# Kernel tuning notes

Hardware: AMD Instinct MI355X
Metric: run time of the kernel (lower is better)

The kernel has to match this reference:

```python
import jax, jax.numpy as jnp
import numpy as np

B, L, H = 32, 512, 1024
H2 = H // 2          # split half = 512
D_ATTN = 64
EPS = 1e-5


def setup_inputs() -> dict:
    key = jax.random.key(0)
    ks = jax.random.split(key, 6)
    x = jax.random.normal(ks[0], (B, L, H), dtype=jnp.float32)
    # LayerNorm params (default torch init: weight=1, bias=0)
    ln_gamma = jnp.ones((H2,), jnp.float32)
    ln_beta = jnp.zeros((H2,), jnp.float32)
    # Toeplitz params (module inits w_vector=0, bias=1; use small random w for nontrivial math)
    w_vector = jax.random.normal(ks[1], (2 * L - 1,), jnp.float32) * 0.02
    t_bias = jnp.ones((L,), jnp.float32)
    # TinyAttention: kqv Linear(H2 -> 3*d_attn), proj Linear(d_attn -> H2)
    kqv_w = jax.random.normal(ks[2], (H2, 3 * D_ATTN), jnp.float32) * 0.02
    kqv_b = jnp.zeros((3 * D_ATTN,), jnp.float32)
    proj_w = jax.random.normal(ks[3], (D_ATTN, H2), jnp.float32) * 0.02
    proj_b = jnp.zeros((H2,), jnp.float32)
    return {"x": x, "ln_gamma": ln_gamma, "ln_beta": ln_beta,
            "w_vector": w_vector, "t_bias": t_bias,
            "kqv_w": kqv_w, "kqv_b": kqv_b, "proj_w": proj_w, "proj_b": proj_b}


def _toeplitz(w_vector):
    # Faithful replication of get_toeplitz(): pad, tile, trim, reshape, crop.
    r = w_vector.shape[0] // 2            # = L - 1
    t = jnp.pad(w_vector, (0, L))         # length 3L - 1
    t = jnp.tile(t, L)[:-L]               # length L * (3L - 2)
    t = t.reshape(L, 3 * L - 2)
    return t[:, r:-r]                      # [L, L]


def _tiny_attention(v, kqv_w, kqv_b, proj_w, proj_b):
    kqv = v @ kqv_w + kqv_b                        # [B, L, 3*d_attn]
    k, q, val = jnp.split(kqv, 3, axis=-1)         # chunk order: key, query, value
    scale = 1.0 / jnp.sqrt(jnp.float32(q.shape[-1]))
    scores = jnp.einsum('bqd,bkd->bqk', q, k) * scale
    soft = jax.nn.softmax(scores, axis=-1)
    head = jnp.einsum('bqk,bkd->bqd', soft, val)   # [B, L, d_attn]
    return head @ proj_w + proj_b                  # [B, L, H2]


def reference(x, ln_gamma, ln_beta, w_vector, t_bias, kqv_w, kqv_b, proj_w, proj_b):
    u, v = jnp.split(x, 2, axis=-1)                # each [B, L, H2]
    head = _tiny_attention(v, kqv_w, kqv_b, proj_w, proj_b)
    # LayerNorm over last dim
    mu = jnp.mean(v, axis=-1, keepdims=True)
    var = jnp.mean(jnp.square(v - mu), axis=-1, keepdims=True)
    vn = (v - mu) * jax.lax.rsqrt(var + EPS) * ln_gamma + ln_beta
    # spatial (Toeplitz) mixing: permute -> [B, H2, L], matmul [L, L], bias
    w_t = _toeplitz(w_vector)
    vm = jnp.einsum('blc,lm->bmc', vn, w_t.T).transpose(0, 2, 1)  # keep faithful: vp @ w_t
    vm = jnp.einsum('bcl,lm->bcm', vn.transpose(0, 2, 1), w_t) + t_bias
    v_out = vm.transpose(0, 2, 1) + head           # [B, L, H2]
    return u * v_out
```

## Files before the change

### kernel.cpp

```cpp
#include <hip/hip_runtime.h>
#include <math.h>

#define NB 32
#define LL 512
#define HH 1024
#define H2 512
#define DA 64

typedef unsigned int u32;
typedef unsigned short u16;
typedef __bf16 bf16x8 __attribute__((ext_vector_type(8)));
typedef float f32x4 __attribute__((ext_vector_type(4)));

__device__ __forceinline__ u16 f2bu(float f) {
    u32 u = __builtin_bit_cast(u32, f);
    u = (u + 0x7fff + ((u >> 16) & 1)) >> 16;
    return (u16)u;
}

__device__ __forceinline__ void async_cp16(const void* g, void* l) {
    __builtin_amdgcn_global_load_lds(
        (const __attribute__((address_space(1))) u32*)g,
        (__attribute__((address_space(3))) u32*)l, 16, 0, 0);
}

__global__ void prep_kernel(const float* __restrict__ wv,
                            const float* __restrict__ kqvw,
                            const float* __restrict__ projw,
                            u16* __restrict__ wt, u16* __restrict__ kqvwT,
                            u16* __restrict__ projwT) {
    int e = blockIdx.x * 256 + threadIdx.x;
    if (e < 262144) {
        int m = e >> 9, l = e & 511;
        wt[e] = f2bu(wv[511 + m - l]);
    } else if (e < 262144 + 98304) {
        int i = e - 262144;
        int n = i >> 9, k = i & 511;
        kqvwT[i] = f2bu(kqvw[(size_t)k * 192 + n]);
    } else {
        int i = e - 360448;
        int c = i >> 6, d = i & 63;
        projwT[i] = f2bu(projw[(size_t)d * 512 + c]);
    }
}

__global__ __launch_bounds__(256, 2)
void front_kernel(const float* __restrict__ x,
                  const float* __restrict__ gamma, const float* __restrict__ beta,
                  const u16* __restrict__ kqvwT, const float* __restrict__ kqvb,
                  u16* __restrict__ vnT,
                  u16* __restrict__ qb, u16* __restrict__ kb, u16* __restrict__ vT) {
    __shared__ u16 smem[64 * 72 + 192 * 64];
    u16* As = smem;
    u16* Bs = smem + 64 * 72;
    u16* T  = Bs;
    int blk = blockIdx.x, t = threadIdx.x;
    int b = blk >> 3, l0 = (blk & 7) * 64;
    int lane = t & 63, wid = t >> 6;
    int l15 = lane & 15, q16 = lane >> 4, q8 = q16 * 8;

    int r = t >> 2, q = t & 3;
    const float* xr = x + ((size_t)(b * LL + l0 + r)) * HH + H2;
    float s1 = 0.0f, s2 = 0.0f;
#pragma unroll
    for (int i = 0; i < 32; ++i) {
        float4 v = *(const float4*)(xr + q * 128 + i * 4);
        s1 += v.x + v.y + v.z + v.w;
        s2 += v.x * v.x + v.y * v.y + v.z * v.z + v.w * v.w;
    }
    s1 += __shfl_xor(s1, 1); s2 += __shfl_xor(s2, 1);
    s1 += __shfl_xor(s1, 2); s2 += __shfl_xor(s2, 2);
    float mu = s1 * (1.0f / H2);
    float rstd = rsqrtf(s2 * (1.0f / H2) - mu * mu + 1e-5f);

    for (int ct = 0; ct < 8; ++ct) {
        int cb = (t & 3) * 16;
#pragma unroll
        for (int i = 0; i < 4; ++i) {
            float4 v = *(const float4*)(xr + ct * 64 + cb + i * 4);
            int c = cb + i * 4;
            T[(c + 0) * 68 + r] = f2bu((v.x - mu) * rstd * gamma[ct * 64 + c + 0] + beta[ct * 64 + c + 0]);
            T[(c + 1) * 68 + r] = f2bu((v.y - mu) * rstd * gamma[ct * 64 + c + 1] + beta[ct * 64 + c + 1]);
            T[(c + 2) * 68 + r] = f2bu((v.z - mu) * rstd * gamma[ct * 64 + c + 2] + beta[ct * 64 + c + 2]);
            T[(c + 3) * 68 + r] = f2bu((v.w - mu) * rstd * gamma[ct * 64 + c + 3] + beta[ct * 64 + c + 3]);
        }
        __syncthreads();
        int c = t >> 2, lo = (t & 3) * 16;
        u16* dst = vnT + ((size_t)(b * H2 + ct * 64 + c)) * LL + l0 + lo;
        const u16* src = T + c * 68 + lo;
        ((ushort4*)dst)[0] = ((const ushort4*)src)[0];
        ((ushort4*)dst)[1] = ((const ushort4*)src)[1];
        ((ushort4*)dst)[2] = ((const ushort4*)src)[2];
        ((ushort4*)dst)[3] = ((const ushort4*)src)[3];
        __syncthreads();
    }

    int wm = (wid & 1) * 32, wn = (wid >> 1) * 96;
    f32x4 acc[2][6] = {};
    for (int k0 = 0; k0 < 512; k0 += 64) {
#pragma unroll
        for (int s = 0; s < 6; ++s) {
            int ci = t + s * 256;
            int grow = ci >> 3, gcol = ((ci & 7) ^ (grow & 7)) << 3;
            async_cp16(kqvwT + (size_t)grow * 512 + k0 + gcol, Bs + ci * 8);
        }
#pragma unroll
        for (int s = 0; s < 4; ++s) {
            int ci = t + s * 256;
            int row = ci >> 4, c4 = (ci & 15) * 4;
            float4 v = *(const float4*)(x + (size_t)(b * LL + l0 + row) * HH + H2 + k0 + c4);
            ushort4 p;
            p.x = f2bu(v.x); p.y = f2bu(v.y); p.z = f2bu(v.z); p.w = f2bu(v.w);
            *(ushort4*)(As + row * 72 + c4) = p;
        }
        __syncthreads();
#pragma unroll
        for (int kk = 0; kk < 2; ++kk) {
            int j0 = kk * 4 + q16;
            bf16x8 a[2];
#pragma unroll
            for (int i = 0; i < 2; ++i)
                a[i] = *(const bf16x8*)(As + (wm + i * 16 + l15) * 72 + kk * 32 + q8);
#pragma unroll
            for (int j = 0; j < 6; ++j) {
                int n = wn + j * 16 + l15;
                bf16x8 bb = *(const bf16x8*)(Bs + (n * 8 + (j0 ^ (n & 7))) * 8);
#pragma unroll
                for (int i = 0; i < 2; ++i)
                    acc[i][j] = __builtin_amdgcn_mfma_f32_16x16x32_bf16(a[i], bb, acc[i][j], 0, 0, 0);
            }
        }
        __syncthreads();
    }
    u16* Ts = Bs;
    int rq = q16 * 4;
#pragma unroll
    for (int i = 0; i < 2; ++i)
#pragma unroll
        for (int rr = 0; rr < 4; ++rr) {
            int mloc = wm + i * 16 + rq + rr;
            size_t mg = (size_t)(b * LL + l0 + mloc);
#pragma unroll
            for (int j = 0; j < 6; ++j) {
                int n = wn + j * 16 + l15;
                u16 hv = f2bu(acc[i][j][rr] + kqvb[n]);
                if (n < 64)       kb[mg * 64 + n] = hv;
                else if (n < 128) qb[mg * 64 + (n - 64)] = hv;
                else              Ts[(n - 128) * 68 + mloc] = hv;
            }
        }
    __syncthreads();
    int d = t >> 2, mo = (t & 3) * 16;
    u16* dst = vT + ((size_t)(b * 64 + d)) * 512 + l0 + mo;
    const u16* srcl = Ts + d * 68 + mo;
#pragma unroll
    for (int c = 0; c < 4; ++c)
        ((ushort4*)dst)[c] = ((const ushort4*)srcl)[c];
}

#define VLD 136
__global__ __launch_bounds__(256, 4)
void attn_kernel(const u16* __restrict__ qb, const u16* __restrict__ kb,
                 const u16* __restrict__ vT, u16* __restrict__ head) {
    __shared__ u16 Ps[4 * 16 * VLD];
    __shared__ float Osh[4][16 * 65];
    __shared__ float Msh[4][16], Lsh[4][16];
    int b = blockIdx.y, q0 = blockIdx.x * 16;
    int t = threadIdx.x, lane = t & 63, w = t >> 6;
    int l15 = lane & 15, q16 = lane >> 4, q8 = q16 * 8;
    int kc = w * 128;
    const u16* qg = qb + (size_t)b * LL * DA;
    const u16* kg = kb + (size_t)b * LL * DA;
    const u16* vg = vT + (size_t)b * DA * LL;

    bf16x8 aq[2];
#pragma unroll
    for (int s = 0; s < 2; ++s)
        aq[s] = *(const bf16x8*)(qg + (size_t)(q0 + l15) * DA + s * 32 + q8);

    f32x4 sc[8] = {};
#pragma unroll
    for (int j = 0; j < 8; ++j) {
#pragma unroll
        for (int s = 0; s < 2; ++s) {
            bf16x8 bk = *(const bf16x8*)(kg + (size_t)(kc + j * 16 + l15) * DA + s * 32 + q8);
            sc[j] = __builtin_amdgcn_mfma_f32_16x16x32_bf16(aq[s], bk, sc[j], 0, 0, 0);
        }
    }
    float mx[4], sm[4];
#pragma unroll
    for (int j = 0; j < 8; ++j)
#pragma unroll
        for (int rr = 0; rr < 4; ++rr) sc[j][rr] *= 0.125f;
#pragma unroll
    for (int rr = 0; rr < 4; ++rr) {
        float m0 = sc[0][rr];
#pragma unroll
        for (int j = 1; j < 8; ++j) m0 = fmaxf(m0, sc[j][rr]);
        m0 = fmaxf(m0, __shfl_xor(m0, 1));
        m0 = fmaxf(m0, __shfl_xor(m0, 2));
        m0 = fmaxf(m0, __shfl_xor(m0, 4));
        m0 = fmaxf(m0, __shfl_xor(m0, 8));
        mx[rr] = m0;
    }
#pragma unroll
    for (int j = 0; j < 8; ++j)
#pragma unroll
        for (int rr = 0; rr < 4; ++rr) sc[j][rr] = __expf(sc[j][rr] - mx[rr]);
#pragma unroll
    for (int rr = 0; rr < 4; ++rr) {
        float s0 = sc[0][rr];
#pragma unroll
        for (int j = 1; j < 8; ++j) s0 += sc[j][rr];
        s0 += __shfl_xor(s0, 1);
        s0 += __shfl_xor(s0, 2);
        s0 += __shfl_xor(s0, 4);
        s0 += __shfl_xor(s0, 8);
        sm[rr] = s0;
    }
    u16* Pw = Ps + w * 16 * VLD;
#pragma unroll
    for (int j = 0; j < 8; ++j)
#pragma unroll
        for (int rr = 0; rr < 4; ++rr)
            Pw[(q16 * 4 + rr) * VLD + j * 16 + l15] = f2bu(sc[j][rr]);
    f32x4 o[4] = {};
#pragma unroll
    for (int kt = 0; kt < 4; ++kt) {
        bf16x8 ap = *(const bf16x8*)(Pw + l15 * VLD + kt * 32 + q8);
#pragma unroll
        for (int j = 0; j < 4; ++j) {
            bf16x8 bv = *(const bf16x8*)(vg + (size_t)(j * 16 + l15) * LL + kc + kt * 32 + q8);
            o[j] = __builtin_amdgcn_mfma_f32_16x16x32_bf16(ap, bv, o[j], 0, 0, 0);
        }
    }
#pragma unroll
    for (int j = 0; j < 4; ++j)
#pragma unroll
        for (int rr = 0; rr < 4; ++rr)
            Osh[w][(q16 * 4 + rr) * 65 + j * 16 + l15] = o[j][rr];
    if (l15 == 0) {
#pragma unroll
        for (int rr = 0; rr < 4; ++rr) {
            Msh[w][q16 * 4 + rr] = mx[rr];
            Lsh[w][q16 * 4 + rr] = sm[rr];
        }
    }
    __syncthreads();
    int qq = t >> 4, dg = (t & 15) * 4;
    float m0 = Msh[0][qq], m1 = Msh[1][qq], m2 = Msh[2][qq], m3 = Msh[3][qq];
    float ms = fmaxf(fmaxf(m0, m1), fmaxf(m2, m3));
    float f0 = __expf(m0 - ms), f1 = __expf(m1 - ms), f2 = __expf(m2 - ms), f3 = __expf(m3 - ms);
    float lst = Lsh[0][qq] * f0 + Lsh[1][qq] * f1 + Lsh[2][qq] * f2 + Lsh[3][qq] * f3;
    float inv = 1.0f / lst;
    ushort4 res;
    u16* rp = (u16*)&res;
#pragma unroll
    for (int i = 0; i < 4; ++i) {
        int idx = qq * 65 + dg + i;
        float a = Osh[0][idx] * f0 + Osh[1][idx] * f1 + Osh[2][idx] * f2 + Osh[3][idx] * f3;
        rp[i] = f2bu(a * inv);
    }
    *(ushort4*)(head + (size_t)(b * LL + q0 + qq) * DA + dg) = res;
}

__device__ __forceinline__ void mfma_tile64(const u16* As, const u16* Bs,
                                            f32x4 acc[4][4], int wm, int wn,
                                            int l15, int q16) {
    int s7 = l15 & 7;
#pragma unroll
    for (int kk = 0; kk < 2; ++kk) {
        int j0 = kk * 4 + q16;
        bf16x8 a[4], bv[4];
#pragma unroll
        for (int i = 0; i < 4; ++i) {
            int row = wm + i * 16 + l15;
            a[i] = *(const bf16x8*)(As + (row * 8 + (j0 ^ s7)) * 8);
        }
#pragma unroll
        for (int j = 0; j < 4; ++j) {
            int row = wn + j * 16 + l15;
            bv[j] = *(const bf16x8*)(Bs + (row * 8 + (j0 ^ s7)) * 8);
        }
#pragma unroll
        for (int i = 0; i < 4; ++i)
#pragma unroll
            for (int j = 0; j < 4; ++j)
                acc[i][j] = __builtin_amdgcn_mfma_f32_16x16x32_bf16(a[i], bv[j], acc[i][j], 0, 0, 0);
    }
}

__global__ __launch_bounds__(256, 2)
void mix_kernel(const u16* __restrict__ wt,
                const u16* __restrict__ vnT,
                const u16* __restrict__ headb,
                const u16* __restrict__ projwT,
                const float* __restrict__ x,
                const float* __restrict__ tbias,
                const float* __restrict__ projb,
                float* __restrict__ out) {
    __shared__ u16 As[128 * 64];
    __shared__ u16 Bs[128 * 64];
    int lid = blockIdx.x;
    int p8 = lid & 7, rest = lid >> 3;
    int mi = rest & 3, pair = (rest >> 2) * 8 + p8;
    int b = pair >> 2, m0 = mi * 128, c0 = (pair & 3) * 128;
    int t = threadIdx.x, lane = t & 63, wid = t >> 6;
    int wm = (wid >> 1) * 64, wn = (wid & 1) * 64;
    int l15 = lane & 15, q16 = lane >> 4;
    f32x4 acc[4][4] = {};
    const u16* Ag = wt + (size_t)m0 * 512;
    const u16* Bg = vnT + ((size_t)b * H2 + c0) * 512;
    for (int k0 = 0; k0 < 512; k0 += 64) {
#pragma unroll
        for (int s = 0; s < 4; ++s) {
            int ci = t + s * 256;
            int grow = ci >> 3, gcol = ((ci & 7) ^ (grow & 7)) << 3;
            async_cp16(Ag + (size_t)grow * 512 + k0 + gcol, As + ci * 8);
            async_cp16(Bg + (size_t)grow * 512 + k0 + gcol, Bs + ci * 8);
        }
        __syncthreads();
        mfma_tile64(As, Bs, acc, wm, wn, l15, q16);
        __syncthreads();
    }
    {
        const u16* Hg = headb + ((size_t)b * LL + m0) * DA;
        const u16* Pg = projwT + (size_t)c0 * DA;
#pragma unroll
        for (int s = 0; s < 4; ++s) {
            int ci = t + s * 256;
            int grow = ci >> 3, gcol = ((ci & 7) ^ (grow & 7)) << 3;
            async_cp16(Hg + (size_t)grow * 64 + gcol, As + ci * 8);
            async_cp16(Pg + (size_t)grow * 64 + gcol, Bs + ci * 8);
        }
        __syncthreads();
        mfma_tile64(As, Bs, acc, wm, wn, l15, q16);
        __syncthreads();
    }
    int rq = q16 * 4;
#pragma unroll
    for (int i = 0; i < 4; ++i) {
#pragma unroll
        for (int rr = 0; rr < 4; ++rr) {
            int m = m0 + wm + i * 16 + rq + rr;
            float tb = tbias[m];
            const float* xrow = x + ((size_t)b * LL + m) * HH;
            float* orow = out + ((size_t)b * LL + m) * H2;
#pragma unroll
            for (int j = 0; j < 4; ++j) {
                int c = c0 + wn + j * 16 + l15;
                float val = acc[i][j][rr] + tb + projb[c];
                orow[c] = xrow[c] * val;
            }
        }
    }
}

extern "C" void kernel_launch(void* const* d_in, const int* in_sizes, int n_in,
                              void* d_out, int out_size, void* d_ws, size_t ws_size,
                              hipStream_t stream) {
    (void)in_sizes; (void)n_in; (void)out_size; (void)ws_size;
    const float* x     = (const float*)d_in[0];
    const float* gamma = (const float*)d_in[1];
    const float* beta  = (const float*)d_in[2];
    const float* wv    = (const float*)d_in[3];
    const float* tb    = (const float*)d_in[4];
    const float* kqvw  = (const float*)d_in[5];
    const float* kqvb  = (const float*)d_in[6];
    const float* projw = (const float*)d_in[7];
    const float* projb = (const float*)d_in[8];
    float* out = (float*)d_out;

    u16* vnT_bf  = (u16*)d_ws;
    u16* qb      = vnT_bf + (size_t)NB * LL * H2;
    u16* kb      = qb + (size_t)NB * LL * DA;
    u16* vTb     = kb + (size_t)NB * LL * DA;
    u16* head_bf = vTb + (size_t)NB * LL * DA;
    u16* wt_bf   = head_bf + (size_t)NB * LL * DA;
    u16* kqvwT   = wt_bf + 512 * 512;
    u16* projwT  = kqvwT + 192 * 512;

    prep_kernel <<<1536, 256, 0, stream>>>(wv, kqvw, projw, wt_bf, kqvwT, projwT);
    front_kernel<<<256, 256, 0, stream>>>(x, gamma, beta, kqvwT, kqvb,
                                          vnT_bf, qb, kb, vTb);
    attn_kernel <<<dim3(32, NB), 256, 0, stream>>>(qb, kb, vTb, head_bf);
    mix_kernel  <<<512, 256, 0, stream>>>(wt_bf, vnT_bf, head_bf, projwT,
                                          x, tb, projb, out);
}
```

Measured before the change: 181.4 us.

## Halve front kernel row tile to 32 and prefetch first weight tile early

The front kernel now handles 32 sequence rows per block instead of 64, doubling the grid to 512 blocks so more of the GPU's compute units get work. Shared memory is split into separate A, B and transpose buffers. This lets the first kqv weight tile be copied asynchronously at kernel start, overlapping with the LayerNorm statistics pass. In exchange each block reloads the full kqv weight matrix for half as many rows, and each wave issues fewer MFMAs per B-fragment load.

```diff
diff --git a/kernel.cpp b/kernel.cpp
--- a/kernel.cpp
+++ b/kernel.cpp
@@ -50,62 +50,72 @@
                   const u16* __restrict__ kqvwT, const float* __restrict__ kqvb,
                   u16* __restrict__ vnT,
                   u16* __restrict__ qb, u16* __restrict__ kb, u16* __restrict__ vT) {
-    __shared__ u16 smem[64 * 72 + 192 * 64];
-    u16* As = smem;
-    u16* Bs = smem + 64 * 72;
-    u16* T  = Bs;
+    __shared__ u16 As[32 * 72];
+    __shared__ u16 Bs[192 * 64];
+    __shared__ u16 T[64 * 36];
     int blk = blockIdx.x, t = threadIdx.x;
-    int b = blk >> 3, l0 = (blk & 7) * 64;
+    int b = blk >> 4, l0 = (blk & 15) * 32;
     int lane = t & 63, wid = t >> 6;
     int l15 = lane & 15, q16 = lane >> 4, q8 = q16 * 8;
 
-    int r = t >> 2, q = t & 3;
+#pragma unroll
+    for (int s = 0; s < 6; ++s) {
+        int ci = t + s * 256;
+        int grow = ci >> 3, gcol = ((ci & 7) ^ (grow & 7)) << 3;
+        async_cp16(kqvwT + (size_t)grow * 512 + gcol, Bs + ci * 8);
+    }
+
+    int r = t >> 3, q = t & 7;
     const float* xr = x + ((size_t)(b * LL + l0 + r)) * HH + H2;
     float s1 = 0.0f, s2 = 0.0f;
 #pragma unroll
-    for (int i = 0; i < 32; ++i) {
-        float4 v = *(const float4*)(xr + q * 128 + i * 4);
+    for (int i = 0; i < 16; ++i) {
+        float4 v = *(const float4*)(xr + q * 64 + i * 4);
         s1 += v.x + v.y + v.z + v.w;
         s2 += v.x * v.x + v.y * v.y + v.z * v.z + v.w * v.w;
     }
     s1 += __shfl_xor(s1, 1); s2 += __shfl_xor(s2, 1);
     s1 += __shfl_xor(s1, 2); s2 += __shfl_xor(s2, 2);
+    s1 += __shfl_xor(s1, 4); s2 += __shfl_xor(s2, 4);
     float mu = s1 * (1.0f / H2);
     float rstd = rsqrtf(s2 * (1.0f / H2) - mu * mu + 1e-5f);
 
+    int c8 = (t & 7) * 8;
     for (int ct = 0; ct < 8; ++ct) {
-        int cb = (t & 3) * 16;
-#pragma unroll
-        for (int i = 0; i < 4; ++i) {
-            float4 v = *(const float4*)(xr + ct * 64 + cb + i * 4);
-            int c = cb + i * 4;
-            T[(c + 0) * 68 + r] = f2bu((v.x - mu) * rstd * gamma[ct * 64 + c + 0] + beta[ct * 64 + c + 0]);
-            T[(c + 1) * 68 + r] = f2bu((v.y - mu) * rstd * gamma[ct * 64 + c + 1] + beta[ct * 64 + c + 1]);
-            T[(c + 2) * 68 + r] = f2bu((v.z - mu) * rstd * gamma[ct * 64 + c + 2] + beta[ct * 64 + c + 2]);
-            T[(c + 3) * 68 + r] = f2bu((v.w - mu) * rstd * gamma[ct * 64 + c + 3] + beta[ct * 64 + c + 3]);
-        }
-        __syncthreads();
-        int c = t >> 2, lo = (t & 3) * 16;
+        float4 v0 = *(const float4*)(xr + ct * 64 + c8);
+        float4 v1 = *(const float4*)(xr + ct * 64 + c8 + 4);
+        const float* g = gamma + ct * 64 + c8;
+        const float* be = beta + ct * 64 + c8;
+        T[(c8 + 0) * 36 + r] = f2bu((v0.x - mu) * rstd * g[0] + be[0]);
+        T[(c8 + 1) * 36 + r] = f2bu((v0.y - mu) * rstd * g[1] + be[1]);
+        T[(c8 + 2) * 36 + r] = f2bu((v0.z - mu) * rstd * g[2] + be[2]);
+        T[(c8 + 3) * 36 + r] = f2bu((v0.w - mu) * rstd * g[3] + be[3]);
+        T[(c8 + 4) * 36 + r] = f2bu((v1.x - mu) * rstd * g[4] + be[4]);
+        T[(c8 + 5) * 36 + r] = f2bu((v1.y - mu) * rstd * g[5] + be[5]);
+        T[(c8 + 6) * 36 + r] = f2bu((v1.z - mu) * rstd * g[6] + be[6]);
+        T[(c8 + 7) * 36 + r] = f2bu((v1.w - mu) * rstd * g[7] + be[7]);
+        __syncthreads();
+        int c = t >> 2, lo = (t & 3) * 8;
         u16* dst = vnT + ((size_t)(b * H2 + ct * 64 + c)) * LL + l0 + lo;
-        const u16* src = T + c * 68 + lo;
+        const u16* src = T + c * 36 + lo;
         ((ushort4*)dst)[0] = ((const ushort4*)src)[0];
         ((ushort4*)dst)[1] = ((const ushort4*)src)[1];
-        ((ushort4*)dst)[2] = ((const ushort4*)src)[2];
-        ((ushort4*)dst)[3] = ((const ushort4*)src)[3];
-        __syncthreads();
-    }
-
-    int wm = (wid & 1) * 32, wn = (wid >> 1) * 96;
-    f32x4 acc[2][6] = {};
+        __syncthreads();
+    }
+
+    int wm = (wid & 1) * 16, wn = (wid >> 1) * 96;
+    f32x4 acc[6] = {};
     for (int k0 = 0; k0 < 512; k0 += 64) {
-#pragma unroll
-        for (int s = 0; s < 6; ++s) {
-            int ci = t + s * 256;
-            int grow = ci >> 3, gcol = ((ci & 7) ^ (grow & 7)) << 3;
-            async_cp16(kqvwT + (size_t)grow * 512 + k0 + gcol, Bs + ci * 8);
-        }
-#pragma unroll
-        for (int s = 0; s < 4; ++s) {
+        if (k0 > 0) {
+#pragma unroll
+            for (int s = 0; s < 6; ++s) {
+                int ci = t + s * 256;
+                int grow = ci >> 3, gcol = ((ci & 7) ^ (grow & 7)) << 3;
+                async_cp16(kqvwT + (size_t)grow * 512 + k0 + gcol, Bs + ci * 8);
+            }
+        }
+#pragma unroll
+        for (int s = 0; s < 2; ++s) {
             int ci = t + s * 256;
             int row = ci >> 4, c4 = (ci & 15) * 4;
             float4 v = *(const float4*)(x + (size_t)(b * LL + l0 + row) * HH + H2 + k0 + c4);
@@ -117,45 +127,37 @@
 #pragma unroll
         for (int kk = 0; kk < 2; ++kk) {
             int j0 = kk * 4 + q16;
-            bf16x8 a[2];
-#pragma unroll
-            for (int i = 0; i < 2; ++i)
-                a[i] = *(const bf16x8*)(As + (wm + i * 16 + l15) * 72 + kk * 32 + q8);
+            bf16x8 a = *(const bf16x8*)(As + (wm + l15) * 72 + kk * 32 + q8);
 #pragma unroll
             for (int j = 0; j < 6; ++j) {
                 int n = wn + j * 16 + l15;
                 bf16x8 bb = *(const bf16x8*)(Bs + (n * 8 + (j0 ^ (n & 7))) * 8);
-#pragma unroll
-                for (int i = 0; i < 2; ++i)
-                    acc[i][j] = __builtin_amdgcn_mfma_f32_16x16x32_bf16(a[i], bb, acc[i][j], 0, 0, 0);
+                acc[j] = __builtin_amdgcn_mfma_f32_16x16x32_bf16(a, bb, acc[j], 0, 0, 0);
             }
         }
         __syncthreads();
     }
-    u16* Ts = Bs;
+    u16* Ts = As;
     int rq = q16 * 4;
 #pragma unroll
-    for (int i = 0; i < 2; ++i)
-#pragma unroll
-        for (int rr = 0; rr < 4; ++rr) {
-            int mloc = wm + i * 16 + rq + rr;
-            size_t mg = (size_t)(b * LL + l0 + mloc);
-#pragma unroll
-            for (int j = 0; j < 6; ++j) {
-                int n = wn + j * 16 + l15;
-                u16 hv = f2bu(acc[i][j][rr] + kqvb[n]);
-                if (n < 64)       kb[mg * 64 + n] = hv;
-                else if (n < 128) qb[mg * 64 + (n - 64)] = hv;
-                else              Ts[(n - 128) * 68 + mloc] = hv;
-            }
-        }
+    for (int rr = 0; rr < 4; ++rr) {
+        int mloc = wm + rq + rr;
+        size_t mg = (size_t)(b * LL + l0 + mloc);
+#pragma unroll
+        for (int j = 0; j < 6; ++j) {
+            int n = wn + j * 16 + l15;
+            u16 hv = f2bu(acc[j][rr] + kqvb[n]);
+            if (n < 64)       kb[mg * 64 + n] = hv;
+            else if (n < 128) qb[mg * 64 + (n - 64)] = hv;
+            else              Ts[(n - 128) * 36 + mloc] = hv;
+        }
+    }
     __syncthreads();
-    int d = t >> 2, mo = (t & 3) * 16;
-    u16* dst = vT + ((size_t)(b * 64 + d)) * 512 + l0 + mo;
-    const u16* srcl = Ts + d * 68 + mo;
-#pragma unroll
-    for (int c = 0; c < 4; ++c)
-        ((ushort4*)dst)[c] = ((const ushort4*)srcl)[c];
+    int d = t >> 2, lo2 = (t & 3) * 8;
+    u16* dst = vT + ((size_t)(b * 64 + d)) * 512 + l0 + lo2;
+    const u16* src = Ts + d * 36 + lo2;
+    ((ushort4*)dst)[0] = ((const ushort4*)src)[0];
+    ((ushort4*)dst)[1] = ((const ushort4*)src)[1];
 }
 
 #define VLD 136
@@ -381,7 +383,7 @@
     u16* projwT  = kqvwT + 192 * 512;
 
     prep_kernel <<<1536, 256, 0, stream>>>(wv, kqvw, projw, wt_bf, kqvwT, projwT);
-    front_kernel<<<256, 256, 0, stream>>>(x, gamma, beta, kqvwT, kqvb,
+    front_kernel<<<512, 256, 0, stream>>>(x, gamma, beta, kqvwT, kqvb,
                                           vnT_bf, qb, kb, vTb);
     attn_kernel <<<dim3(32, NB), 256, 0, stream>>>(qb, kb, vTb, head_bf);
     mix_kernel  <<<512, 256, 0, stream>>>(wt_bf, vnT_bf, head_bf, projwT,
```

Measured after the change: 176.3 us. 2.8% less time.
